# Performance work log

Measured on AMD Instinct MI355X. Metric: run time of the kernel, lower is better.

Reference implementation:

```python
import jax, jax.numpy as jnp
import numpy as np

D_MODEL, N_LAYERS, D_INNER, D_STATE, D_CONV, DT_RANK, NUM_CLASSES = 256, 4, 512, 16, 4, 16, 10
B, L = 8, 1024


def setup_inputs() -> dict:
    key = jax.random.key(0)
    ks = jax.random.split(key, 16)
    s = 0.02
    inp = {}
    inp['x'] = jax.random.normal(ks[0], (B, L, 1), jnp.float32)
    inp['input_w'] = jax.random.normal(ks[1], (D_MODEL, 1), jnp.float32) * s
    inp['input_b'] = jnp.zeros((D_MODEL,), jnp.float32)
    inp['ln_w'] = jnp.ones((N_LAYERS, D_MODEL), jnp.float32)
    inp['ln_b'] = jnp.zeros((N_LAYERS, D_MODEL), jnp.float32)
    inp['in_proj_w'] = jax.random.normal(ks[2], (N_LAYERS, 2 * D_INNER, D_MODEL), jnp.float32) * s
    inp['in_proj_b'] = jnp.zeros((N_LAYERS, 2 * D_INNER), jnp.float32)
    inp['conv_w'] = jax.random.normal(ks[3], (N_LAYERS, D_INNER, 1, D_CONV), jnp.float32) * 0.2
    inp['conv_b'] = jnp.zeros((N_LAYERS, D_INNER), jnp.float32)
    inp['x_proj_w'] = jax.random.normal(ks[4], (N_LAYERS, DT_RANK + 2 * D_STATE, D_INNER), jnp.float32) * s
    inp['dt_proj_w'] = jax.random.normal(ks[5], (N_LAYERS, D_INNER, DT_RANK), jnp.float32) * s
    inp['dt_proj_b'] = jax.random.normal(ks[6], (N_LAYERS, D_INNER), jnp.float32) * 0.1 - 4.0  # small softplus(dt)
    # canonical S4D-real init: A = [1..d_state] repeated over d_inner
    A = jnp.tile(jnp.arange(1, D_STATE + 1, dtype=jnp.float32)[None, :], (D_INNER, 1))
    inp['A_log'] = jnp.tile(jnp.log(A)[None], (N_LAYERS, 1, 1))
    inp['D'] = jnp.ones((N_LAYERS, D_INNER), jnp.float32)
    inp['out_proj_w'] = jax.random.normal(ks[7], (N_LAYERS, D_MODEL, D_INNER), jnp.float32) * s
    inp['out_proj_b'] = jnp.zeros((N_LAYERS, D_MODEL), jnp.float32)
    inp['norm_w'] = jnp.ones((D_MODEL,), jnp.float32)
    inp['norm_b'] = jnp.zeros((D_MODEL,), jnp.float32)
    inp['cls_w'] = jax.random.normal(ks[8], (NUM_CLASSES, D_MODEL), jnp.float32) * s
    inp['cls_b'] = jnp.zeros((NUM_CLASSES,), jnp.float32)
    return inp


def _layernorm(x, w, b, eps=1e-5):
    mu = jnp.mean(x, axis=-1, keepdims=True)
    var = jnp.mean(jnp.square(x - mu), axis=-1, keepdims=True)
    return (x - mu) * jax.lax.rsqrt(var + eps) * w + b


def _causal_depthwise_conv(u, w, b):
    # u: (B, L, D_inner), w: (D_inner, 1, K), causal padding K-1
    out = jax.lax.conv_general_dilated(
        u.transpose(0, 2, 1), w, window_strides=(1,), padding=[(D_CONV - 1, 0)],
        feature_group_count=D_INNER, dimension_numbers=('NCH', 'OIH', 'NCH'))
    return out.transpose(0, 2, 1) + b


def _selective_scan(u, delta, A, Bm, Cm, Dp):
    # u, delta: (B,L,Din); Bm, Cm: (B,L,N); A: (Din,N); Dp: (Din,)
    def step(h, inp):
        d_t, B_t, C_t, u_t = inp                       # (B,Din),(B,N),(B,N),(B,Din)
        dA = jnp.exp(d_t[:, :, None] * A)              # (B,Din,N)
        dBu = d_t[:, :, None] * B_t[:, None, :] * u_t[:, :, None]
        h = dA * h + dBu
        y = jnp.einsum('bdn,bn->bd', h, C_t)
        return h, y
    h0 = jnp.zeros((u.shape[0], D_INNER, D_STATE), u.dtype)
    xs = (delta.transpose(1, 0, 2), Bm.transpose(1, 0, 2), Cm.transpose(1, 0, 2), u.transpose(1, 0, 2))
    _, ys = jax.lax.scan(step, h0, xs)                 # ys: (L,B,Din)
    return ys.transpose(1, 0, 2) + u * Dp


def _mamba_layer(x, ln_w, ln_b, ipw, ipb, cw, cb, xpw, dtw, dtb, A_log, Dp, opw, opb):
    h = _layernorm(x, ln_w, ln_b)
    xz = jnp.einsum('bld,ed->ble', h, ipw) + ipb       # (B,L,2*Din)
    u, res = jnp.split(xz, 2, axis=-1)
    u = jax.nn.silu(_causal_depthwise_conv(u, cw, cb))
    x_dbl = jnp.einsum('bld,ed->ble', u, xpw)          # (B,L,dt_rank+2N)
    dt, Bm, Cm = jnp.split(x_dbl, [DT_RANK, DT_RANK + D_STATE], axis=-1)
    delta = jax.nn.softplus(jnp.einsum('blr,dr->bld', dt, dtw) + dtb)
    A = -jnp.exp(A_log)
    y = _selective_scan(u, delta, A, Bm, Cm, Dp)
    y = y * jax.nn.silu(res)
    return x + jnp.einsum('ble,de->bld', y, opw) + opb


def reference(x, input_w, input_b, ln_w, ln_b, in_proj_w, in_proj_b, conv_w, conv_b,
              x_proj_w, dt_proj_w, dt_proj_b, A_log, D, out_proj_w, out_proj_b,
              norm_w, norm_b, cls_w, cls_b):
    h = jnp.einsum('blc,dc->bld', x, input_w) + input_b   # (B,L,D_MODEL)
    for i in range(N_LAYERS):
        h = _mamba_layer(h, ln_w[i], ln_b[i], in_proj_w[i], in_proj_b[i], conv_w[i], conv_b[i],
                         x_proj_w[i], dt_proj_w[i], dt_proj_b[i], A_log[i], D[i],
                         out_proj_w[i], out_proj_b[i])
    h = _layernorm(h, norm_w, norm_b)
    pooled = jnp.mean(h, axis=1)                          # (B, D_MODEL)
    return jnp.einsum('bd,cd->bc', pooled, cls_w) + cls_b
```

## Files before the change

kernel.cpp:

```cpp
#include <hip/hip_runtime.h>
#include <hip/hip_bf16.h>
#include <math.h>

#define DM 256
#define NL 4
#define DI 512
#define DS 16
#define DC 4
#define DR 16
#define NC 10
#define NB 8
#define LL 1024
#define MR (NB*LL)
#define NCHUNK 64
#define CLEN 16

typedef __attribute__((ext_vector_type(4))) float f32x4;
typedef __attribute__((ext_vector_type(8))) short short8;

extern "C" __device__ float __ocml_native_exp2_f32(float);
__device__ __forceinline__ float exp2_f(float x) { return __ocml_native_exp2_f32(x); }
#define L2E 1.442695040888963f

__device__ __forceinline__ float silu_f(float x) {
    return x * (1.0f / (1.0f + __expf(-x)));
}
__device__ __forceinline__ float bf2f(ushort v) {
    union { unsigned u; float f; } c; c.u = ((unsigned)v) << 16; return c.f;
}
__device__ __forceinline__ ushort f2bf(float f) {
    union { float f; unsigned u; } c; c.f = f;
    unsigned lsb = (c.u >> 16) & 1;
    return (ushort)((c.u + 0x7fffu + lsb) >> 16);
}
__device__ __forceinline__ void g2lds16(const void* g, void* l) {
    __builtin_amdgcn_global_load_lds((const __attribute__((address_space(1))) void*)g,
                                     (__attribute__((address_space(3))) void*)l, 16, 0, 0);
}

#define IPW_N (NL*2*DI*DM)
#define XPW_N (NL*64*DI)
#define OPW_N (NL*DM*DI)
#define AV_N  (NL*DI*DS)
__global__ __launch_bounds__(256) void convert_weights_kernel(
        const float* __restrict__ ipw, const float* __restrict__ xpw,
        const float* __restrict__ opw, const float* __restrict__ A_log,
        ushort* __restrict__ ipw_b, ushort* __restrict__ xpw_b,
        ushort* __restrict__ opw_b, float* __restrict__ Av) {
    int t = blockIdx.x * 256 + threadIdx.x;
    if (t < IPW_N) { ipw_b[t] = f2bf(ipw[t]); return; }
    t -= IPW_N;
    if (t < XPW_N) {
        int l = t >> 15, r = (t >> 9) & 63, k = t & 511;
        xpw_b[t] = (r < 48) ? f2bf(xpw[((size_t)l * 48 + r) * DI + k]) : (ushort)0;
        return;
    }
    t -= XPW_N;
    if (t < OPW_N) { opw_b[t] = f2bf(opw[t]); return; }
    t -= OPW_N;
    if (t < AV_N) Av[t] = -__expf(A_log[t]) * L2E;
}

__global__ __launch_bounds__(256) void input_ln_kernel(
        const float* __restrict__ x, const float* __restrict__ iw,
        const float* __restrict__ ib,
        const float* __restrict__ lnw, const float* __restrict__ lnb,
        float* __restrict__ hres, ushort* __restrict__ hln) {
    int row = blockIdx.x, t = threadIdx.x;
    float v = x[row] * iw[t] + ib[t];
    float s = v, q = v * v;
#pragma unroll
    for (int o = 32; o >= 1; o >>= 1) { s += __shfl_xor(s, o); q += __shfl_xor(q, o); }
    __shared__ float red[8];
    int wid = t >> 6;
    if ((t & 63) == 0) { red[wid] = s; red[4 + wid] = q; }
    __syncthreads();
    s = red[0] + red[1] + red[2] + red[3];
    q = red[4] + red[5] + red[6] + red[7];
    float mu = s * (1.0f / DM);
    float var = q * (1.0f / DM) - mu * mu;
    float rs = rsqrtf(var + 1e-5f);
    hres[row * DM + t] = v;
    hln[row * DM + t] = f2bf((v - mu) * rs * lnw[t] + lnb[t]);
}

template<int BM, int BN, int WM, int WN, int MODE>
__global__ __launch_bounds__(256) void mfma_gemm_kernel(
        const ushort* __restrict__ A, int lda,
        const ushort* __restrict__ W,
        const float* __restrict__ bias,
        ushort* __restrict__ Cb, float* __restrict__ Cf, int ldc, int K) {
    constexpr int FM = BM / WM / 16;
    constexpr int FN = BN / WN / 16;
    __shared__ __align__(16) char smem[(BM + BN) * 128];
    const int tid = threadIdx.x;
    const int l = tid & 63, w = tid >> 6;
    const int wr = w / WN, wc = w % WN;
    const int bm = blockIdx.x * BM, bn = blockIdx.y * BN;
    const int ldw = K;

    f32x4 acc[FM][FN] = {};

    for (int k0 = 0; k0 < K; k0 += 64) {
#pragma unroll
        for (int i = 0; i < (BM * 128 / 16) / 256; i++) {
            int lin = (i * 256 + tid) * 16;
            int q = lin ^ (((lin >> 7) & 7) << 4);
            g2lds16(A + (size_t)(bm + (q >> 7)) * lda + k0 + ((q & 127) >> 1), smem + lin);
        }
#pragma unroll
        for (int i = 0; i < (BN * 128 / 16) / 256; i++) {
            int lin = (i * 256 + tid) * 16;
            int q = lin ^ (((lin >> 7) & 7) << 4);
            g2lds16(W + (size_t)(bn + (q >> 7)) * ldw + k0 + ((q & 127) >> 1),
                    smem + BM * 128 + lin);
        }
        __syncthreads();
        const int rl = l & 15;
        const int kb0 = ((l >> 4) << 3) * 2;
#pragma unroll
        for (int kk = 0; kk < 2; kk++) {
            short8 af[FM], bfr[FN];
#pragma unroll
            for (int m = 0; m < FM; m++) {
                int off = (wr * (BM / WM) + m * 16 + rl) * 128 + kk * 64 + kb0;
                off ^= ((off >> 7) & 7) << 4;
                af[m] = *(const short8*)(smem + off);
            }
#pragma unroll
            for (int n = 0; n < FN; n++) {
                int off = (wc * (BN / WN) + n * 16 + rl) * 128 + kk * 64 + kb0;
                off ^= ((off >> 7) & 7) << 4;
                bfr[n] = *(const short8*)(smem + BM * 128 + off);
            }
#pragma unroll
            for (int m = 0; m < FM; m++)
#pragma unroll
                for (int n = 0; n < FN; n++)
                    acc[m][n] = __builtin_amdgcn_mfma_f32_16x16x32_bf16(
                        af[m], bfr[n], acc[m][n], 0, 0, 0);
        }
        __syncthreads();
    }

    const int row0 = bm + wr * (BM / WM) + ((l >> 4) << 2);
    const int col0 = bn + wc * (BN / WN) + (l & 15);
#pragma unroll
    for (int m = 0; m < FM; m++) {
#pragma unroll
        for (int n = 0; n < FN; n++) {
            int col = col0 + n * 16;
            float bv = (MODE == 1) ? 0.f : bias[col];
#pragma unroll
            for (int r = 0; r < 4; r++) {
                size_t idx = (size_t)(row0 + m * 16 + r) * ldc + col;
                float v = acc[m][n][r];
                if (MODE == 0) Cb[idx] = f2bf(v + bv);
                else Cf[idx] = v;
            }
        }
    }
}

__global__ __launch_bounds__(256) void outproj_ln_kernel(
        const ushort* __restrict__ A,
        const ushort* __restrict__ W,
        const float* __restrict__ bias,
        float* __restrict__ hres,
        const float* __restrict__ lnw, const float* __restrict__ lnb,
        ushort* __restrict__ hln) {
    constexpr int K = DI;
    __shared__ __align__(16) char smem[(16 + 256) * 128];
    const int tid = threadIdx.x;
    const int l = tid & 63, w = tid >> 6;
    const int bm = blockIdx.x * 16;

    f32x4 acc[4] = {};

    for (int k0 = 0; k0 < K; k0 += 64) {
        if (tid < 128) {
            int lin = tid * 16;
            int q = lin ^ (((lin >> 7) & 7) << 4);
            g2lds16(A + (size_t)(bm + (q >> 7)) * K + k0 + ((q & 127) >> 1), smem + lin);
        }
#pragma unroll
        for (int i = 0; i < 8; i++) {
            int lin = (i * 256 + tid) * 16;
            int q = lin ^ (((lin >> 7) & 7) << 4);
            g2lds16(W + (size_t)(q >> 7) * K + k0 + ((q & 127) >> 1), smem + 16 * 128 + lin);
        }
        __syncthreads();
        const int rl = l & 15;
        const int kb0 = ((l >> 4) << 3) * 2;
#pragma unroll
        for (int kk = 0; kk < 2; kk++) {
            short8 af;
            {
                int off = rl * 128 + kk * 64 + kb0;
                off ^= ((off >> 7) & 7) << 4;
                af = *(const short8*)(smem + off);
            }
            short8 bfr[4];
#pragma unroll
            for (int n = 0; n < 4; n++) {
                int off = (w * 64 + n * 16 + rl) * 128 + kk * 64 + kb0;
                off ^= ((off >> 7) & 7) << 4;
                bfr[n] = *(const short8*)(smem + 16 * 128 + off);
            }
#pragma unroll
            for (int n = 0; n < 4; n++)
                acc[n] = __builtin_amdgcn_mfma_f32_16x16x32_bf16(af, bfr[n], acc[n], 0, 0, 0);
        }
        __syncthreads();
    }

    const int r0 = (l >> 4) << 2;
    const int col0 = w * 64 + (l & 15);
    float vv[4][4];
    float s[4], q[4];
#pragma unroll
    for (int r = 0; r < 4; r++) { s[r] = 0.f; q[r] = 0.f; }
#pragma unroll
    for (int n = 0; n < 4; n++) {
        int col = col0 + n * 16;
        float bv = bias[col];
#pragma unroll
        for (int r = 0; r < 4; r++) {
            int row = bm + r0 + r;
            float x = acc[n][r] + bv + hres[(size_t)row * DM + col];
            vv[n][r] = x;
            s[r] += x;
            q[r] += x * x;
        }
    }
#pragma unroll
    for (int o = 1; o < 16; o <<= 1) {
#pragma unroll
        for (int r = 0; r < 4; r++) {
            s[r] += __shfl_xor(s[r], o);
            q[r] += __shfl_xor(q[r], o);
        }
    }
    float* red  = (float*)smem;
    float* redq = red + 64;
    if ((l & 15) == 0) {
#pragma unroll
        for (int r = 0; r < 4; r++) {
            int rl2 = r0 + r;
            red[rl2 * 4 + w] = s[r];
            redq[rl2 * 4 + w] = q[r];
        }
    }
    __syncthreads();
    float mu[4], rs[4];
#pragma unroll
    for (int r = 0; r < 4; r++) {
        int rl2 = r0 + r;
        float ts = red[rl2 * 4] + red[rl2 * 4 + 1] + red[rl2 * 4 + 2] + red[rl2 * 4 + 3];
        float tq = redq[rl2 * 4] + redq[rl2 * 4 + 1] + redq[rl2 * 4 + 2] + redq[rl2 * 4 + 3];
        mu[r] = ts * (1.0f / DM);
        float var = tq * (1.0f / DM) - mu[r] * mu[r];
        rs[r] = rsqrtf(var + 1e-5f);
    }
#pragma unroll
    for (int n = 0; n < 4; n++) {
        int col = col0 + n * 16;
        float lw = lnw[col], lb = lnb[col];
#pragma unroll
        for (int r = 0; r < 4; r++) {
            int row = bm + r0 + r;
            hres[(size_t)row * DM + col] = vv[n][r];
            hln[(size_t)row * DM + col] = f2bf((vv[n][r] - mu[r]) * rs[r] * lw + lb);
        }
    }
}

__global__ __launch_bounds__(256) void conv_silu_kernel(const ushort* __restrict__ xz,
        const float* __restrict__ cw, const float* __restrict__ cb, ushort* __restrict__ u) {
    int t = blockIdx.x * 256 + threadIdx.x;
    int d8 = (t & 63) << 3;
    int m = t >> 6;
    int l = m & (LL - 1);
    const short8 zr = {0, 0, 0, 0, 0, 0, 0, 0};
    const size_t base = (size_t)m * 1024 + d8;
    short8 r3 = *(const short8*)(xz + base);
    short8 r2 = (l >= 1) ? *(const short8*)(xz + base - 1024) : zr;
    short8 r1 = (l >= 2) ? *(const short8*)(xz + base - 2048) : zr;
    short8 r0 = (l >= 3) ? *(const short8*)(xz + base - 3072) : zr;
    short8 o;
#pragma unroll
    for (int j = 0; j < 8; j++) {
        int d = d8 + j;
        float4 w4 = *reinterpret_cast<const float4*>(&cw[d * 4]);
        float a = cb[d] + w4.w * bf2f((ushort)r3[j]);
        a += w4.z * bf2f((ushort)r2[j]);
        a += w4.y * bf2f((ushort)r1[j]);
        a += w4.x * bf2f((ushort)r0[j]);
        o[j] = (short)f2bf(silu_f(a));
    }
    *(short8*)(u + (size_t)m * DI + d8) = o;
}

__global__ __launch_bounds__(256, 4) void scan_phase1_kernel(
        const ushort* __restrict__ u, const float* __restrict__ x_dbl,
        const float* __restrict__ Av,
        const float* __restrict__ dtw, const float* __restrict__ dtb,
        const float* __restrict__ Dp,
        float* __restrict__ sdv, float* __restrict__ Sbuf,
        unsigned* __restrict__ cy) {
    __shared__ __align__(16) float xs[CLEN * 64];
    const int tid = threadIdx.x;
    const int bc = blockIdx.x >> 1;
    const int d = ((blockIdx.x & 1) << 8) + tid;
    const int c = bc & (NCHUNK - 1);
    const int b = bc >> 6;
    const int m0 = b * LL + c * CLEN;
    *reinterpret_cast<float4*>(&xs[tid * 4]) =
        *reinterpret_cast<const float4*>(&x_dbl[(size_t)m0 * 64 + tid * 4]);

    float Aval[DS], h[DS], wreg[DR];
#pragma unroll
    for (int q = 0; q < 4; q++) {
        float4 a4 = *reinterpret_cast<const float4*>(&Av[d * DS + q * 4]);
        Aval[q*4+0] = a4.x; Aval[q*4+1] = a4.y; Aval[q*4+2] = a4.z; Aval[q*4+3] = a4.w;
        float4 w4 = *reinterpret_cast<const float4*>(&dtw[d * DR + q * 4]);
        wreg[q*4] = w4.x; wreg[q*4+1] = w4.y; wreg[q*4+2] = w4.z; wreg[q*4+3] = w4.w;
    }
    float dbv = dtb[d];
    float Dval = Dp[d];
#pragma unroll
    for (int n = 0; n < DS; n++) h[n] = 0.f;
    const ushort* up = u + (size_t)m0 * DI + d;
    unsigned* cyp = cy + (size_t)m0 * DI + d;
    float sd = 0.f;
    __syncthreads();
    float uv = bf2f(up[0]);
    for (int t = 0; t < CLEN; t++) {
        float uvn = (t + 1 < CLEN) ? bf2f(up[(size_t)(t + 1) * DI]) : 0.f;
        const float* xr = &xs[t * 64];
        float4 x0 = *reinterpret_cast<const float4*>(xr);
        float4 x1 = *reinterpret_cast<const float4*>(xr + 4);
        float4 x2 = *reinterpret_cast<const float4*>(xr + 8);
        float4 x3 = *reinterpret_cast<const float4*>(xr + 12);
        float4 B0 = *reinterpret_cast<const float4*>(xr + 16);
        float4 B1 = *reinterpret_cast<const float4*>(xr + 20);
        float4 B2 = *reinterpret_cast<const float4*>(xr + 24);
        float4 B3 = *reinterpret_cast<const float4*>(xr + 28);
        float4 C0 = *reinterpret_cast<const float4*>(xr + 32);
        float4 C1 = *reinterpret_cast<const float4*>(xr + 36);
        float4 C2 = *reinterpret_cast<const float4*>(xr + 40);
        float4 C3 = *reinterpret_cast<const float4*>(xr + 44);
        float p0 = dbv + wreg[0]*x0.x + wreg[1]*x0.y + wreg[2]*x0.z + wreg[3]*x0.w;
        float p1 = wreg[4]*x1.x + wreg[5]*x1.y + wreg[6]*x1.z + wreg[7]*x1.w;
        float p2 = wreg[8]*x2.x + wreg[9]*x2.y + wreg[10]*x2.z + wreg[11]*x2.w;
        float p3 = wreg[12]*x3.x + wreg[13]*x3.y + wreg[14]*x3.z + wreg[15]*x3.w;
        float z = (p0 + p1) + (p2 + p3);
        float dv = (z > 20.0f) ? z : __logf(1.0f + __expf(z));
        sd += dv;
        float du = dv * uv;
        float a0, a1, a2, a3;
        h[0]  = exp2_f(dv*Aval[0])  * h[0]  + du * B0.x;  a0  = h[0]  * C0.x;
        h[1]  = exp2_f(dv*Aval[1])  * h[1]  + du * B0.y;  a0 += h[1]  * C0.y;
        h[2]  = exp2_f(dv*Aval[2])  * h[2]  + du * B0.z;  a0 += h[2]  * C0.z;
        h[3]  = exp2_f(dv*Aval[3])  * h[3]  + du * B0.w;  a0 += h[3]  * C0.w;
        h[4]  = exp2_f(dv*Aval[4])  * h[4]  + du * B1.x;  a1  = h[4]  * C1.x;
        h[5]  = exp2_f(dv*Aval[5])  * h[5]  + du * B1.y;  a1 += h[5]  * C1.y;
        h[6]  = exp2_f(dv*Aval[6])  * h[6]  + du * B1.z;  a1 += h[6]  * C1.z;
        h[7]  = exp2_f(dv*Aval[7])  * h[7]  + du * B1.w;  a1 += h[7]  * C1.w;
        h[8]  = exp2_f(dv*Aval[8])  * h[8]  + du * B2.x;  a2  = h[8]  * C2.x;
        h[9]  = exp2_f(dv*Aval[9])  * h[9]  + du * B2.y;  a2 += h[9]  * C2.y;
        h[10] = exp2_f(dv*Aval[10]) * h[10] + du * B2.z;  a2 += h[10] * C2.z;
        h[11] = exp2_f(dv*Aval[11]) * h[11] + du * B2.w;  a2 += h[11] * C2.w;
        h[12] = exp2_f(dv*Aval[12]) * h[12] + du * B3.x;  a3  = h[12] * C3.x;
        h[13] = exp2_f(dv*Aval[13]) * h[13] + du * B3.y;  a3 += h[13] * C3.y;
        h[14] = exp2_f(dv*Aval[14]) * h[14] + du * B3.z;  a3 += h[14] * C3.z;
        h[15] = exp2_f(dv*Aval[15]) * h[15] + du * B3.w;  a3 += h[15] * C3.w;
        float yv = ((a0 + a1) + (a2 + a3)) + Dval * uv;
        cyp[(size_t)t * DI] = (unsigned)f2bf(sd) | ((unsigned)f2bf(yv) << 16);
        uv = uvn;
    }
    size_t base = ((size_t)((b * NCHUNK + c) * DI + d)) * DS;
#pragma unroll
    for (int q = 0; q < 4; q++)
        *reinterpret_cast<float4*>(&Sbuf[base + q * 4]) =
            make_float4(h[q*4], h[q*4+1], h[q*4+2], h[q*4+3]);
    sdv[(b * NCHUNK + c) * DI + d] = sd;
}

__global__ __launch_bounds__(256) void scan_phase2_kernel(
        const float* __restrict__ sdv, const float* __restrict__ Av,
        float* __restrict__ Sbuf) {
    int gid = blockIdx.x * 256 + threadIdx.x;
    int dn = gid & (DI * DS - 1);
    int b = gid >> 13;
    int n = dn & 15, d = dn >> 4;
    float Aval = Av[d * DS + n];
    size_t idx0 = (size_t)b * NCHUNK * DI * DS + dn;
    const size_t stride = (size_t)DI * DS;
    int sb0 = b * NCHUNK * DI + d;
    float h = 0.f;
    float S0[8], sd0[8];
#pragma unroll
    for (int j = 0; j < 8; j++) {
        S0[j] = Sbuf[idx0 + (size_t)j * stride];
        sd0[j] = sdv[sb0 + j * DI];
    }
    for (int g = 0; g < NCHUNK / 8; g++) {
        float S1[8], sd1[8];
        if (g < NCHUNK / 8 - 1) {
            int c1 = g * 8 + 8;
#pragma unroll
            for (int j = 0; j < 8; j++) {
                S1[j] = Sbuf[idx0 + (size_t)(c1 + j) * stride];
                sd1[j] = sdv[sb0 + (c1 + j) * DI];
            }
        } else {
#pragma unroll
            for (int j = 0; j < 8; j++) { S1[j] = 0.f; sd1[j] = 0.f; }
        }
#pragma unroll
        for (int j = 0; j < 8; j++) {
            float P = exp2_f(Aval * sd0[j]);
            Sbuf[idx0 + (size_t)(g * 8 + j) * stride] = h;
            h = P * h + S0[j];
        }
#pragma unroll
        for (int j = 0; j < 8; j++) { S0[j] = S1[j]; sd0[j] = sd1[j]; }
    }
}

__global__ __launch_bounds__(256, 4) void scan_phase3_kernel(
        const unsigned* __restrict__ cy,
        const float* __restrict__ x_dbl, const float* __restrict__ Av,
        const float* __restrict__ Sbuf,
        const ushort* __restrict__ xz, ushort* __restrict__ y) {
    __shared__ __align__(16) float cs[CLEN * 16];
    const int tid = threadIdx.x;
    const int bc = blockIdx.x >> 1;
    const int d = ((blockIdx.x & 1) << 8) + tid;
    const int c = bc & (NCHUNK - 1);
    const int b = bc >> 6;
    const int m0 = b * LL + c * CLEN;
    {
        int tt = tid >> 4, k = tid & 15;
        cs[tt * 16 + k] = x_dbl[(size_t)(m0 + tt) * 64 + 32 + k];
    }
    float Aval[DS], hi[DS];
    size_t base = ((size_t)((b * NCHUNK + c) * DI + d)) * DS;
#pragma unroll
    for (int q = 0; q < 4; q++) {
        float4 a4 = *reinterpret_cast<const float4*>(&Av[d * DS + q * 4]);
        Aval[q*4+0] = a4.x; Aval[q*4+1] = a4.y; Aval[q*4+2] = a4.z; Aval[q*4+3] = a4.w;
        float4 h4 = *reinterpret_cast<const float4*>(&Sbuf[base + q * 4]);
        hi[q*4] = h4.x; hi[q*4+1] = h4.y; hi[q*4+2] = h4.z; hi[q*4+3] = h4.w;
    }
    const unsigned* cyp = cy + (size_t)m0 * DI + d;
    const ushort* rp = xz + (size_t)m0 * 1024 + 512 + d;
    ushort* yp = y + (size_t)m0 * DI + d;
    __syncthreads();
    unsigned cyw = cyp[0];
    float rv = bf2f(rp[0]);
#pragma unroll 4
    for (int t = 0; t < CLEN; t++) {
        unsigned cywn = 0; float rvn = 0.f;
        if (t + 1 < CLEN) {
            cywn = cyp[(size_t)(t + 1) * DI];
            rvn = bf2f(rp[(size_t)(t + 1) * 1024]);
        }
        float cd = bf2f((ushort)(cyw & 0xffffu));
        float yl = bf2f((ushort)(cyw >> 16));
        const float* cr = &cs[t * 16];
        float4 C0 = *reinterpret_cast<const float4*>(cr);
        float4 C1 = *reinterpret_cast<const float4*>(cr + 4);
        float4 C2 = *reinterpret_cast<const float4*>(cr + 8);
        float4 C3 = *reinterpret_cast<const float4*>(cr + 12);
        float a0, a1, a2, a3;
        a0  = exp2_f(Aval[0]  * cd) * hi[0]  * C0.x;
        a0 += exp2_f(Aval[1]  * cd) * hi[1]  * C0.y;
        a0 += exp2_f(Aval[2]  * cd) * hi[2]  * C0.z;
        a0 += exp2_f(Aval[3]  * cd) * hi[3]  * C0.w;
        a1  = exp2_f(Aval[4]  * cd) * hi[4]  * C1.x;
        a1 += exp2_f(Aval[5]  * cd) * hi[5]  * C1.y;
        a1 += exp2_f(Aval[6]  * cd) * hi[6]  * C1.z;
        a1 += exp2_f(Aval[7]  * cd) * hi[7]  * C1.w;
        a2  = exp2_f(Aval[8]  * cd) * hi[8]  * C2.x;
        a2 += exp2_f(Aval[9]  * cd) * hi[9]  * C2.y;
        a2 += exp2_f(Aval[10] * cd) * hi[10] * C2.z;
        a2 += exp2_f(Aval[11] * cd) * hi[11] * C2.w;
        a3  = exp2_f(Aval[12] * cd) * hi[12] * C3.x;
        a3 += exp2_f(Aval[13] * cd) * hi[13] * C3.y;
        a3 += exp2_f(Aval[14] * cd) * hi[14] * C3.z;
        a3 += exp2_f(Aval[15] * cd) * hi[15] * C3.w;
        float yv = yl + ((a0 + a1) + (a2 + a3));
        yp[(size_t)t * DI] = f2bf(yv * silu_f(rv));
        cyw = cywn; rv = rvn;
    }
}

__global__ __launch_bounds__(256) void pool_partial_kernel(const ushort* __restrict__ ln,
                                                           float* __restrict__ partial) {
    int bs = blockIdx.x;
    int b = bs >> 3, sl = bs & 7;
    int t = threadIdx.x;
    int l0 = sl * 128;
    float s = 0.f;
    for (int l = 0; l < 128; l++) s += bf2f(ln[(size_t)(b * LL + l0 + l) * DM + t]);
    partial[(bs << 8) + t] = s;
}

__global__ void cls_kernel(const float* __restrict__ partial, const float* __restrict__ cw,
                           const float* __restrict__ cb, float* __restrict__ out) {
    int t = threadIdx.x;
    if (t >= NB * NC) return;
    int b = t / NC, c = t % NC;
    float s = 0.f;
    for (int k = 0; k < DM; k++) {
        float p = 0.f;
#pragma unroll
        for (int sl = 0; sl < 8; sl++) p += partial[((b * 8 + sl) << 8) + k];
        s += p * cw[c * DM + k];
    }
    out[t] = cb[c] + s * (1.0f / LL);
}

extern "C" void kernel_launch(void* const* d_in, const int* in_sizes, int n_in,
                              void* d_out, int out_size, void* d_ws, size_t ws_size,
                              hipStream_t stream) {
    const float* x       = (const float*)d_in[0];
    const float* input_w = (const float*)d_in[1];
    const float* input_b = (const float*)d_in[2];
    const float* ln_w    = (const float*)d_in[3];
    const float* ln_b    = (const float*)d_in[4];
    const float* ipw     = (const float*)d_in[5];
    const float* ipb     = (const float*)d_in[6];
    const float* cw      = (const float*)d_in[7];
    const float* cb      = (const float*)d_in[8];
    const float* xpw     = (const float*)d_in[9];
    const float* dtw     = (const float*)d_in[10];
    const float* dtb     = (const float*)d_in[11];
    const float* A_log   = (const float*)d_in[12];
    const float* Dp      = (const float*)d_in[13];
    const float* opw     = (const float*)d_in[14];
    const float* opb     = (const float*)d_in[15];
    const float* norm_w  = (const float*)d_in[16];
    const float* norm_b  = (const float*)d_in[17];
    const float* cls_w   = (const float*)d_in[18];
    const float* cls_b   = (const float*)d_in[19];
    float* out = (float*)d_out;
    float* ws = (float*)d_ws;

    float*    hres   = ws;
    ushort*   xz     = (ushort*)(hres + (size_t)MR * DM);
    ushort*   ub     = xz + (size_t)MR * 1024;
    float*    x_dbl  = (float*)(ub + (size_t)MR * DI);
    float*    sdvb   = x_dbl + (size_t)MR * 64;
    float*    Sbuf   = sdvb + (size_t)NB * NCHUNK * DI;
    float*    partial= Sbuf + (size_t)NB * NCHUNK * DI * DS;
    ushort*   ygate  = (ushort*)(partial + 64 * 256);
    ushort*   hln    = ygate + (size_t)MR * DI;
    ushort*   ipw_b  = hln + (size_t)MR * DM;
    ushort*   xpw_b  = ipw_b + IPW_N;
    ushort*   opw_b  = xpw_b + XPW_N;
    float*    Avbuf  = (float*)(opw_b + OPW_N);
    unsigned* cy     = (unsigned*)(Avbuf + AV_N);

    convert_weights_kernel<<<(IPW_N + XPW_N + OPW_N + AV_N) / 256, 256, 0, stream>>>(
        ipw, xpw, opw, A_log, ipw_b, xpw_b, opw_b, Avbuf);
    input_ln_kernel<<<MR, 256, 0, stream>>>(x, input_w, input_b, ln_w, ln_b, hres, hln);

    for (int i = 0; i < NL; i++) {
        mfma_gemm_kernel<128, 128, 2, 2, 0><<<dim3(MR / 128, 1024 / 128), 256, 0, stream>>>(
            hln, DM, ipw_b + (size_t)i * 2 * DI * DM, ipb + (size_t)i * 2 * DI,
            xz, nullptr, 1024, DM);
        conv_silu_kernel<<<MR * DI / 8 / 256, 256, 0, stream>>>(xz, cw + i * DI * DC, cb + i * DI, ub);
        mfma_gemm_kernel<32, 64, 2, 2, 1><<<dim3(MR / 32, 1), 256, 0, stream>>>(
            ub, DI, xpw_b + (size_t)i * 64 * DI, nullptr, nullptr, x_dbl, 64, DI);
        scan_phase1_kernel<<<NB * NCHUNK * 2, 256, 0, stream>>>(
            ub, x_dbl, Avbuf + (size_t)i * DI * DS, dtw + i * DI * DR, dtb + i * DI,
            Dp + i * DI, sdvb, Sbuf, cy);
        scan_phase2_kernel<<<NB * DI * DS / 256, 256, 0, stream>>>(
            sdvb, Avbuf + (size_t)i * DI * DS, Sbuf);
        scan_phase3_kernel<<<NB * NCHUNK * 2, 256, 0, stream>>>(
            cy, x_dbl, Avbuf + (size_t)i * DI * DS, Sbuf, xz, ygate);
        const float* nlw = (i < NL - 1) ? (ln_w + (i + 1) * DM) : norm_w;
        const float* nlb = (i < NL - 1) ? (ln_b + (i + 1) * DM) : norm_b;
        outproj_ln_kernel<<<MR / 16, 256, 0, stream>>>(
            ygate, opw_b + (size_t)i * DM * DI, opb + (size_t)i * DM,
            hres, nlw, nlb, hln);
    }

    pool_partial_kernel<<<64, 256, 0, stream>>>(hln, partial);
    cls_kernel<<<1, 128, 0, stream>>>(partial, cls_w, cls_b, out);
}
```

Baseline: 413.2 us.

## Fuse causal conv+SiLU into the x_proj GEMM A-tile load

Removes the standalone conv_silu kernel and computes the depthwise causal conv plus SiLU while loading the A tile of the x_proj GEMM, writing u to global (still needed by the scan) and to swizzled LDS for the MFMAs. This saves one launch and the global re-read of u by the GEMM. In exchange, the conv is computed inside the GEMM's k-loop with 4 row reads of xz per element, and only 256 blocks run, so the conv arithmetic sits on the GEMM's critical path with less parallelism than the old elementwise kernel.

Result: no change. 411.2 us (-0.5%).

```diff
diff --git a/kernel.cpp b/kernel.cpp
--- a/kernel.cpp
+++ b/kernel.cpp
@@ -162,6 +162,91 @@
     }
 }
 
+__global__ __launch_bounds__(256) void xproj_conv_kernel(
+        const ushort* __restrict__ xz,
+        const float* __restrict__ cw,
+        const float* __restrict__ cb,
+        const ushort* __restrict__ W,
+        ushort* __restrict__ u,
+        float* __restrict__ Cf) {
+    constexpr int BM = 32, BN = 64, K = DI;
+    __shared__ __align__(16) char smem[(BM + BN) * 128];
+    const int tid = threadIdx.x;
+    const int l = tid & 63, w = tid >> 6;
+    const int wr = w >> 1, wc = w & 1;
+    const int bm = blockIdx.x * BM;
+    const short8 zr = {0, 0, 0, 0, 0, 0, 0, 0};
+
+    f32x4 acc[2] = {};
+
+    for (int k0 = 0; k0 < K; k0 += 64) {
+        {
+            int row = tid >> 3, grp = tid & 7;
+            int gcol = k0 + grp * 8;
+            size_t base = (size_t)(bm + row) * 1024 + gcol;
+            int lrow = (bm + row) & (LL - 1);
+            short8 r3 = *(const short8*)(xz + base);
+            short8 r2 = (lrow >= 1) ? *(const short8*)(xz + base - 1024) : zr;
+            short8 r1 = (lrow >= 2) ? *(const short8*)(xz + base - 2048) : zr;
+            short8 r0 = (lrow >= 3) ? *(const short8*)(xz + base - 3072) : zr;
+            short8 o;
+#pragma unroll
+            for (int j = 0; j < 8; j++) {
+                int dd = gcol + j;
+                float4 w4 = *reinterpret_cast<const float4*>(&cw[dd * 4]);
+                float a = cb[dd] + w4.w * bf2f((ushort)r3[j])
+                        + w4.z * bf2f((ushort)r2[j])
+                        + w4.y * bf2f((ushort)r1[j])
+                        + w4.x * bf2f((ushort)r0[j]);
+                o[j] = (short)f2bf(silu_f(a));
+            }
+            *(short8*)(u + (size_t)(bm + row) * DI + gcol) = o;
+            int off = row * 128 + grp * 16;
+            off ^= ((off >> 7) & 7) << 4;
+            *(short8*)(smem + off) = o;
+        }
+#pragma unroll
+        for (int i = 0; i < 2; i++) {
+            int lin = (i * 256 + tid) * 16;
+            int q = lin ^ (((lin >> 7) & 7) << 4);
+            g2lds16(W + (size_t)(q >> 7) * K + k0 + ((q & 127) >> 1),
+                    smem + BM * 128 + lin);
+        }
+        __syncthreads();
+        const int rl = l & 15;
+        const int kb0 = ((l >> 4) << 3) * 2;
+#pragma unroll
+        for (int kk = 0; kk < 2; kk++) {
+            short8 af;
+            {
+                int off = (wr * 16 + rl) * 128 + kk * 64 + kb0;
+                off ^= ((off >> 7) & 7) << 4;
+                af = *(const short8*)(smem + off);
+            }
+            short8 bfr[2];
+#pragma unroll
+            for (int n = 0; n < 2; n++) {
+                int off = (wc * 32 + n * 16 + rl) * 128 + kk * 64 + kb0;
+                off ^= ((off >> 7) & 7) << 4;
+                bfr[n] = *(const short8*)(smem + BM * 128 + off);
+            }
+#pragma unroll
+            for (int n = 0; n < 2; n++)
+                acc[n] = __builtin_amdgcn_mfma_f32_16x16x32_bf16(af, bfr[n], acc[n], 0, 0, 0);
+        }
+        __syncthreads();
+    }
+    const int row0 = bm + wr * 16 + ((l >> 4) << 2);
+    const int col0 = wc * 32 + (l & 15);
+#pragma unroll
+    for (int n = 0; n < 2; n++) {
+        int col = col0 + n * 16;
+#pragma unroll
+        for (int r = 0; r < 4; r++)
+            Cf[(size_t)(row0 + r) * 64 + col] = acc[n][r];
+    }
+}
+
 __global__ __launch_bounds__(256) void outproj_ln_kernel(
         const ushort* __restrict__ A,
         const ushort* __restrict__ W,
@@ -273,32 +358,6 @@
             hln[(size_t)row * DM + col] = f2bf((vv[n][r] - mu[r]) * rs[r] * lw + lb);
         }
     }
-}
-
-__global__ __launch_bounds__(256) void conv_silu_kernel(const ushort* __restrict__ xz,
-        const float* __restrict__ cw, const float* __restrict__ cb, ushort* __restrict__ u) {
-    int t = blockIdx.x * 256 + threadIdx.x;
-    int d8 = (t & 63) << 3;
-    int m = t >> 6;
-    int l = m & (LL - 1);
-    const short8 zr = {0, 0, 0, 0, 0, 0, 0, 0};
-    const size_t base = (size_t)m * 1024 + d8;
-    short8 r3 = *(const short8*)(xz + base);
-    short8 r2 = (l >= 1) ? *(const short8*)(xz + base - 1024) : zr;
-    short8 r1 = (l >= 2) ? *(const short8*)(xz + base - 2048) : zr;
-    short8 r0 = (l >= 3) ? *(const short8*)(xz + base - 3072) : zr;
-    short8 o;
-#pragma unroll
-    for (int j = 0; j < 8; j++) {
-        int d = d8 + j;
-        float4 w4 = *reinterpret_cast<const float4*>(&cw[d * 4]);
-        float a = cb[d] + w4.w * bf2f((ushort)r3[j]);
-        a += w4.z * bf2f((ushort)r2[j]);
-        a += w4.y * bf2f((ushort)r1[j]);
-        a += w4.x * bf2f((ushort)r0[j]);
-        o[j] = (short)f2bf(silu_f(a));
-    }
-    *(short8*)(u + (size_t)m * DI + d8) = o;
 }
 
 __global__ __launch_bounds__(256, 4) void scan_phase1_kernel(
@@ -572,9 +631,8 @@
         mfma_gemm_kernel<128, 128, 2, 2, 0><<<dim3(MR / 128, 1024 / 128), 256, 0, stream>>>(
             hln, DM, ipw_b + (size_t)i * 2 * DI * DM, ipb + (size_t)i * 2 * DI,
             xz, nullptr, 1024, DM);
-        conv_silu_kernel<<<MR * DI / 8 / 256, 256, 0, stream>>>(xz, cw + i * DI * DC, cb + i * DI, ub);
-        mfma_gemm_kernel<32, 64, 2, 2, 1><<<dim3(MR / 32, 1), 256, 0, stream>>>(
-            ub, DI, xpw_b + (size_t)i * 64 * DI, nullptr, nullptr, x_dbl, 64, DI);
+        xproj_conv_kernel<<<MR / 32, 256, 0, stream>>>(
+            xz, cw + i * DI * DC, cb + i * DI, xpw_b + (size_t)i * 64 * DI, ub, x_dbl);
         scan_phase1_kernel<<<NB * NCHUNK * 2, 256, 0, stream>>>(
             ub, x_dbl, Avbuf + (size_t)i * DI * DS, dtw + i * DI * DR, dtb + i * DI,
             Dp + i * DI, sdvb, Sbuf, cy);
```
